# Performance work log

Hardware: AMD Instinct MI355X
Metric: run time of the kernel (lower is better)

The kernel has to match this reference:

```python
import jax, jax.numpy as jnp
import numpy as np

A_DIM, V_DIM, L_DIM, H = 512, 768, 1024, 512
B, S = 16, 2048


def setup_inputs() -> dict:
    key = jax.random.key(0)
    ks = jax.random.split(key, 20)
    w = lambda k, shp: jax.random.normal(k, shp, dtype=jnp.float32) * 0.02
    return {
        "a_input": jax.random.normal(ks[0], (B, S, A_DIM), dtype=jnp.float32),
        "v_input": jax.random.normal(ks[1], (B, S, V_DIM), dtype=jnp.float32),
        "l_input": jax.random.normal(ks[2], (B, S, L_DIM), dtype=jnp.float32),
        "h0": jax.random.normal(ks[3], (1, B, H), dtype=jnp.float32),
        "c0": jax.random.normal(ks[4], (1, B, H), dtype=jnp.float32),
        # 1x1 Conv1d == per-timestep Linear: weight [H, in_dim], bias [H]
        "Wa": w(ks[5], (H, A_DIM)), "ba": w(ks[6], (H,)),
        "Wv": w(ks[7], (H, V_DIM)), "bv": w(ks[8], (H,)),
        "Wl": w(ks[9], (H, L_DIM)), "bl": w(ks[10], (H,)),
        "Wc": w(ks[11], (H, 3 * H)), "bc": w(ks[12], (H,)),
        # LSTM params, PyTorch gate order (i, f, g, o)
        "Wih": w(ks[13], (4 * H, H)), "Whh": w(ks[14], (4 * H, H)),
        "bih": w(ks[15], (4 * H,)), "bhh": w(ks[16], (4 * H,)),
    }


def _lstm(x, h0, c0, Wih, Whh, bih, bhh):
    # x: [B, S, H]; h0/c0: [B, H]
    def step(carry, xt):
        h, c = carry
        gates = xt @ Wih.T + bih + h @ Whh.T + bhh  # [B, 4H]
        i, f, g, o = jnp.split(gates, 4, axis=-1)
        c = jax.nn.sigmoid(f) * c + jax.nn.sigmoid(i) * jnp.tanh(g)
        h = jax.nn.sigmoid(o) * jnp.tanh(c)
        return (h, c), h
    (hT, cT), hs = jax.lax.scan(step, (h0, c0), x.transpose(1, 0, 2))
    return hs.transpose(1, 0, 2), hT, cT  # [B,S,H], [B,H], [B,H]


def reference(a_input, v_input, l_input, h0, c0, Wa, ba, Wv, bv, Wl, bl,
              Wc, bc, Wih, Whh, bih, bhh):
    # 1x1 conv projections -> [B, S, H]
    a = a_input @ Wa.T + ba
    v = v_input @ Wv.T + bv
    l = l_input @ Wl.T + bl
    # attention fusion
    context = jnp.tanh(jnp.concatenate([a, v, l], axis=-1) @ Wc.T + bc)  # [B,S,H]
    scores = jnp.stack([
        jnp.sum(a * context, axis=-1),
        jnp.sum(v * context, axis=-1),
        jnp.sum(l * context, axis=-1),
    ], axis=-1)  # [B, S, 3]
    weight = jax.nn.softmax(scores, axis=-1)[..., None]  # [B,S,3,1]
    data = jnp.stack([a, v, l], axis=-2)  # [B,S,3,H]
    fusion = jnp.sum(data * weight, axis=-2)  # [B,S,H]
    r_out, hT, cT = _lstm(fusion, h0[0], c0[0], Wih, Whh, bih, bhh)
    return r_out, hT[None], cT[None]
```

## Files before the change

kernel.cpp:

```cpp
#include <hip/hip_runtime.h>
#include <stdint.h>

#define B_ 16
#define S_ 2048
#define H_ 512
#define M_ (B_ * S_)

template <int ACT>
__global__ __launch_bounds__(256) void gemm_xwt(
    const float* __restrict__ X, const float* __restrict__ W,
    const float* __restrict__ b1, const float* __restrict__ b2,
    float* __restrict__ Y, int K, int ldy)
{
  __shared__ float As[16][132];
  __shared__ float Bs[16][132];
  const int tid = threadIdx.x;
  const int bm = blockIdx.x, bn = blockIdx.y;
  const int ty = tid >> 4, tx = tid & 15;
  const int lr = tid >> 2, lk = (tid & 3) << 2;
  const float* Xb = X + (size_t)(bm * 128) * K;
  const float* Wb = W + (size_t)(bn * 128) * K;

  float acc[8][8] = {};

  for (int k0 = 0; k0 < K; k0 += 16) {
    float4 xa0 = *(const float4*)(Xb + (size_t)lr * K + k0 + lk);
    float4 xa1 = *(const float4*)(Xb + (size_t)(lr + 64) * K + k0 + lk);
    float4 wa0 = *(const float4*)(Wb + (size_t)lr * K + k0 + lk);
    float4 wa1 = *(const float4*)(Wb + (size_t)(lr + 64) * K + k0 + lk);
    __syncthreads();
    As[lk + 0][lr] = xa0.x; As[lk + 1][lr] = xa0.y; As[lk + 2][lr] = xa0.z; As[lk + 3][lr] = xa0.w;
    As[lk + 0][lr + 64] = xa1.x; As[lk + 1][lr + 64] = xa1.y; As[lk + 2][lr + 64] = xa1.z; As[lk + 3][lr + 64] = xa1.w;
    Bs[lk + 0][lr] = wa0.x; Bs[lk + 1][lr] = wa0.y; Bs[lk + 2][lr] = wa0.z; Bs[lk + 3][lr] = wa0.w;
    Bs[lk + 0][lr + 64] = wa1.x; Bs[lk + 1][lr + 64] = wa1.y; Bs[lk + 2][lr + 64] = wa1.z; Bs[lk + 3][lr + 64] = wa1.w;
    __syncthreads();
#pragma unroll
    for (int kk = 0; kk < 16; ++kk) {
      float4 a0 = *(const float4*)&As[kk][ty * 8];
      float4 a1 = *(const float4*)&As[kk][ty * 8 + 4];
      float4 b0 = *(const float4*)&Bs[kk][tx * 8];
      float4 b1v = *(const float4*)&Bs[kk][tx * 8 + 4];
      float av[8] = {a0.x, a0.y, a0.z, a0.w, a1.x, a1.y, a1.z, a1.w};
      float bv[8] = {b0.x, b0.y, b0.z, b0.w, b1v.x, b1v.y, b1v.z, b1v.w};
#pragma unroll
      for (int i = 0; i < 8; ++i)
#pragma unroll
        for (int j = 0; j < 8; ++j) acc[i][j] += av[i] * bv[j];
    }
  }

  const int ncol0 = bn * 128 + tx * 8;
  float bias[8];
#pragma unroll
  for (int j = 0; j < 8; ++j) {
    float bb = b1[ncol0 + j];
    if (b2) bb += b2[ncol0 + j];
    bias[j] = bb;
  }
#pragma unroll
  for (int i = 0; i < 8; ++i) {
    size_t row = (size_t)bm * 128 + ty * 8 + i;
    float* yp = Y + row * (size_t)ldy + ncol0;
    float out[8];
#pragma unroll
    for (int j = 0; j < 8; ++j) {
      float v = acc[i][j] + bias[j];
      if (ACT) v = tanhf(v);
      out[j] = v;
    }
    *(float4*)(yp)     = make_float4(out[0], out[1], out[2], out[3]);
    *(float4*)(yp + 4) = make_float4(out[4], out[5], out[6], out[7]);
  }
}

__global__ __launch_bounds__(256) void fusion_kernel(
    const float* __restrict__ F,
    const float* __restrict__ CTX,
    float* __restrict__ FU)
{
  const int row = blockIdx.x * 4 + (threadIdx.x >> 6);
  const int lane = threadIdx.x & 63;
  const float* a = F + (size_t)row * 1536;
  const float* v = a + 512;
  const float* l = a + 1024;
  const float* c = CTX + (size_t)row * 512;
  float sa = 0.f, sv = 0.f, sl = 0.f;
  for (int k = lane; k < 512; k += 64) {
    float cv = c[k];
    sa += a[k] * cv; sv += v[k] * cv; sl += l[k] * cv;
  }
#pragma unroll
  for (int off = 1; off < 64; off <<= 1) {
    sa += __shfl_xor(sa, off);
    sv += __shfl_xor(sv, off);
    sl += __shfl_xor(sl, off);
  }
  float m = fmaxf(sa, fmaxf(sv, sl));
  float ea = expf(sa - m), ev = expf(sv - m), el = expf(sl - m);
  float inv = 1.0f / (ea + ev + el);
  float wa = ea * inv, wv = ev * inv, wl = el * inv;
  float* fu = FU + (size_t)row * 512;
  for (int k = lane; k < 512; k += 64)
    fu[k] = wa * a[k] + wv * v[k] + wl * l[k];
}

__global__ __launch_bounds__(256, 1) void lstm_kernel(
    const float* __restrict__ G,
    const float* __restrict__ Whh,
    const float* __restrict__ h0,
    const float* __restrict__ c0,
    unsigned long long* __restrict__ ring,
    float* __restrict__ r_out,
    float* __restrict__ hT,
    float* __restrict__ cT)
{
  const int bi = blockIdx.x;
  const int b  = ((bi & 7) << 1) | ((bi >> 3) & 1);
  const int wg = bi >> 4;
  const int k0h = wg << 5;
  const int tid = threadIdx.x;

  __shared__ float h_lds[512];
  __shared__ float gates_lds[128];
  __shared__ float c_lds[32];

  const int col = tid >> 1;
  const int khalf = tid & 1;
  const int kbase = khalf << 8;
  const int g = col >> 5, ul = col & 31;
  const int gcol = g * 512 + k0h + ul;

  float4 warr[64];
  const float* wsrc = Whh + (size_t)gcol * 512 + kbase;
#pragma unroll
  for (int j = 0; j < 64; ++j) warr[j] = *(const float4*)(wsrc + j * 4);

  if (tid < 32) c_lds[tid] = c0[b * H_ + k0h + tid];
  __syncthreads();

  const float* gbase = G + (size_t)b * S_ * 2048;

  for (int t = 0; t < S_; ++t) {
    float gval = 0.f;
    if (khalf == 0) gval = gbase[(size_t)t * 2048 + gcol];

    if (t > 0) {
      const unsigned int want = (unsigned int)(t - 1);
      const unsigned long long* slot =
          ring + ((size_t)((t - 1) & 3) * B_ + b) * H_;
      unsigned long long v0, v1;
      do {
        v0 = __hip_atomic_load(slot + tid, __ATOMIC_RELAXED,
                               __HIP_MEMORY_SCOPE_AGENT);
      } while ((unsigned int)(v0 >> 32) != want);
      do {
        v1 = __hip_atomic_load(slot + tid + 256, __ATOMIC_RELAXED,
                               __HIP_MEMORY_SCOPE_AGENT);
      } while ((unsigned int)(v1 >> 32) != want);
      h_lds[tid]       = __builtin_bit_cast(float, (unsigned int)v0);
      h_lds[tid + 256] = __builtin_bit_cast(float, (unsigned int)v1);
    } else {
      const float* hsrc = h0 + b * H_;
      h_lds[tid] = hsrc[tid];
      h_lds[tid + 256] = hsrc[tid + 256];
    }
    __syncthreads();

    float4 s4 = make_float4(0.f, 0.f, 0.f, 0.f);
#pragma unroll
    for (int j = 0; j < 64; ++j) {
      float4 hv = *(const float4*)&h_lds[kbase + (j << 2)];
      s4.x += warr[j].x * hv.x;
      s4.y += warr[j].y * hv.y;
      s4.z += warr[j].z * hv.z;
      s4.w += warr[j].w * hv.w;
    }
    float sum = (s4.x + s4.y) + (s4.z + s4.w);
    sum += __shfl_xor(sum, 1);
    if (khalf == 0) gates_lds[col] = sum + gval;
    __syncthreads();

    if (tid < 32) {
      const int u = tid;
      float ip = gates_lds[u], fp = gates_lds[32 + u];
      float gp = gates_lds[64 + u], op = gates_lds[96 + u];
      float ig = 1.f / (1.f + expf(-ip));
      float fg = 1.f / (1.f + expf(-fp));
      float gg = tanhf(gp);
      float og = 1.f / (1.f + expf(-op));
      float cn = fg * c_lds[u] + ig * gg;
      c_lds[u] = cn;
      float hn = og * tanhf(cn);
      unsigned long long pk =
          ((unsigned long long)(unsigned int)t << 32) |
          (unsigned long long)__builtin_bit_cast(unsigned int, hn);
      __hip_atomic_store(ring + ((size_t)(t & 3) * B_ + b) * H_ + k0h + u,
                         pk, __ATOMIC_RELAXED, __HIP_MEMORY_SCOPE_AGENT);
      r_out[((size_t)b * S_ + t) * H_ + k0h + u] = hn;
      if (t == S_ - 1) {
        hT[b * H_ + k0h + u] = hn;
        cT[b * H_ + k0h + u] = cn;
      }
    }
    __syncthreads();
  }
}

extern "C" void kernel_launch(void* const* d_in, const int* in_sizes, int n_in,
                              void* d_out, int out_size, void* d_ws, size_t ws_size,
                              hipStream_t stream)
{
  const float* a_in = (const float*)d_in[0];
  const float* v_in = (const float*)d_in[1];
  const float* l_in = (const float*)d_in[2];
  const float* h0   = (const float*)d_in[3];
  const float* c0   = (const float*)d_in[4];
  const float* Wa = (const float*)d_in[5];   const float* ba = (const float*)d_in[6];
  const float* Wv = (const float*)d_in[7];   const float* bv = (const float*)d_in[8];
  const float* Wl = (const float*)d_in[9];   const float* bl = (const float*)d_in[10];
  const float* Wc = (const float*)d_in[11];  const float* bc = (const float*)d_in[12];
  const float* Wih = (const float*)d_in[13]; const float* Whh = (const float*)d_in[14];
  const float* bih = (const float*)d_in[15]; const float* bhh = (const float*)d_in[16];

  char* ws = (char*)d_ws;
  float* Fbuf = (float*)ws;
  float* Gbuf = (float*)ws;
  float* CTX  = (float*)(ws + 268435456ull);
  float* FU   = (float*)(ws + 335544320ull);
  unsigned long long* ringp = (unsigned long long*)(ws + 402653184ull);

  dim3 blk(256);
  gemm_xwt<0><<<dim3(256, 4), blk, 0, stream>>>(a_in, Wa, ba, nullptr, Fbuf + 0,    512,  1536);
  gemm_xwt<0><<<dim3(256, 4), blk, 0, stream>>>(v_in, Wv, bv, nullptr, Fbuf + 512,  768,  1536);
  gemm_xwt<0><<<dim3(256, 4), blk, 0, stream>>>(l_in, Wl, bl, nullptr, Fbuf + 1024, 1024, 1536);
  gemm_xwt<1><<<dim3(256, 4), blk, 0, stream>>>(Fbuf, Wc, bc, nullptr, CTX, 1536, 512);
  fusion_kernel<<<dim3(8192), blk, 0, stream>>>(Fbuf, CTX, FU);
  gemm_xwt<0><<<dim3(256, 16), blk, 0, stream>>>(FU, Wih, bih, bhh, Gbuf, 512, 2048);
  float* out = (float*)d_out;
  lstm_kernel<<<dim3(256), blk, 0, stream>>>(Gbuf, Whh, h0, c0, ringp,
                                             out, out + 16777216ull,
                                             out + 16777216ull + 8192ull);
}
```

Measured before the change: 10.92 ms.

## Rewrite LSTM recurrence with bf16 split-precision MFMA across 32 workgroups

```diff
diff --git a/kernel.cpp b/kernel.cpp
--- a/kernel.cpp
+++ b/kernel.cpp
@@ -5,6 +5,15 @@
 #define S_ 2048
 #define H_ 512
 #define M_ (B_ * S_)
+
+typedef short short8 __attribute__((ext_vector_type(8)));
+typedef float floatx4 __attribute__((ext_vector_type(4)));
+
+static __device__ __forceinline__ unsigned short f2bf(float x) {
+  unsigned u = __builtin_bit_cast(unsigned, x);
+  unsigned r = (u + 0x7fffu + ((u >> 16) & 1u)) >> 16;
+  return (unsigned short)r;
+}
 
 template <int ACT>
 __global__ __launch_bounds__(256) void gemm_xwt(
@@ -74,8 +83,7 @@
 }
 
 __global__ __launch_bounds__(256) void fusion_kernel(
-    const float* __restrict__ F,
-    const float* __restrict__ CTX,
+    const float* __restrict__ F, const float* __restrict__ CTX,
     float* __restrict__ FU)
 {
   const int row = blockIdx.x * 4 + (threadIdx.x >> 6);
@@ -114,95 +122,130 @@
     float* __restrict__ hT,
     float* __restrict__ cT)
 {
-  const int bi = blockIdx.x;
-  const int b  = ((bi & 7) << 1) | ((bi >> 3) & 1);
-  const int wg = bi >> 4;
-  const int k0h = wg << 5;
+  const int wg = blockIdx.x;
+  const int u0 = wg << 4;
   const int tid = threadIdx.x;
-
-  __shared__ float h_lds[512];
-  __shared__ float gates_lds[128];
-  __shared__ float c_lds[32];
-
-  const int col = tid >> 1;
-  const int khalf = tid & 1;
-  const int kbase = khalf << 8;
-  const int g = col >> 5, ul = col & 31;
-  const int gcol = g * 512 + k0h + ul;
-
-  float4 warr[64];
-  const float* wsrc = Whh + (size_t)gcol * 512 + kbase;
-#pragma unroll
-  for (int j = 0; j < 64; ++j) warr[j] = *(const float4*)(wsrc + j * 4);
-
-  if (tid < 32) c_lds[tid] = c0[b * H_ + k0h + tid];
-  __syncthreads();
-
-  const float* gbase = G + (size_t)b * S_ * 2048;
+  const int w = tid >> 6;
+  const int lane = tid & 63;
+  const int mn = lane & 15;
+  const int kq = lane >> 4;
+
+  __shared__ unsigned int h_u32[16 * 260];
+  __shared__ float g_lds[4][16][17];
+
+  short8 wh[16], wl[16];
+  {
+    const float* wrow = Whh + (size_t)(w * 512 + u0 + mn) * 512;
+#pragma unroll
+    for (int kt = 0; kt < 16; ++kt) {
+      const float* p = wrow + kt * 32 + kq * 8;
+      float4 x0 = *(const float4*)p;
+      float4 x1 = *(const float4*)(p + 4);
+      float xs[8] = {x0.x, x0.y, x0.z, x0.w, x1.x, x1.y, x1.z, x1.w};
+      short8 hi, lo;
+#pragma unroll
+      for (int j = 0; j < 8; ++j) {
+        unsigned short hb = f2bf(xs[j]);
+        float hf = __builtin_bit_cast(float, (unsigned)hb << 16);
+        hi[j] = (short)hb;
+        lo[j] = (short)f2bf(xs[j] - hf);
+      }
+      wh[kt] = hi;
+      wl[kt] = lo;
+    }
+  }
+
+  const int pu = tid >> 4, pb = tid & 15;
+  float c_reg = c0[pb * H_ + u0 + pu];
+
+  const int b7 = tid >> 5;
+  const int Ub = (tid & 31) * 16;
 
   for (int t = 0; t < S_; ++t) {
-    float gval = 0.f;
-    if (khalf == 0) gval = gbase[(size_t)t * 2048 + gcol];
-
-    if (t > 0) {
-      const unsigned int want = (unsigned int)(t - 1);
-      const unsigned long long* slot =
-          ring + ((size_t)((t - 1) & 3) * B_ + b) * H_;
-      unsigned long long v0, v1;
+    floatx4 acc0, acc1 = {0,0,0,0}, acc2 = {0,0,0,0}, acc3 = {0,0,0,0};
+    {
+      const size_t gb = ((size_t)mn * S_ + t) * 2048 + (size_t)(w * 512 + u0 + kq * 4);
+#pragma unroll
+      for (int r = 0; r < 4; ++r) acc0[r] = G[gb + r];
+    }
+
+    if (t == 0) {
+      const int sb = tid >> 4, sk = (tid & 15) * 32;
+      const float* hp = h0 + sb * H_ + sk;
+      unsigned int* dst = &h_u32[sb * 260 + sk / 2];
+#pragma unroll
+      for (int i = 0; i < 8; ++i) {
+        float4 x = *(const float4*)(hp + i * 4);
+        dst[i * 2]     = (unsigned)f2bf(x.x) | ((unsigned)f2bf(x.y) << 16);
+        dst[i * 2 + 1] = (unsigned)f2bf(x.z) | ((unsigned)f2bf(x.w) << 16);
+      }
+    } else {
+      const unsigned want = (unsigned)(t - 1);
+      const unsigned long long* slot = ring + (size_t)((t - 1) & 3) * 4096;
+      unsigned long long v[16];
+      bool ok;
       do {
-        v0 = __hip_atomic_load(slot + tid, __ATOMIC_RELAXED,
-                               __HIP_MEMORY_SCOPE_AGENT);
-      } while ((unsigned int)(v0 >> 32) != want);
-      do {
-        v1 = __hip_atomic_load(slot + tid + 256, __ATOMIC_RELAXED,
-                               __HIP_MEMORY_SCOPE_AGENT);
-      } while ((unsigned int)(v1 >> 32) != want);
-      h_lds[tid]       = __builtin_bit_cast(float, (unsigned int)v0);
-      h_lds[tid + 256] = __builtin_bit_cast(float, (unsigned int)v1);
-    } else {
-      const float* hsrc = h0 + b * H_;
-      h_lds[tid] = hsrc[tid];
-      h_lds[tid + 256] = hsrc[tid + 256];
-    }
-    __syncthreads();
-
-    float4 s4 = make_float4(0.f, 0.f, 0.f, 0.f);
-#pragma unroll
-    for (int j = 0; j < 64; ++j) {
-      float4 hv = *(const float4*)&h_lds[kbase + (j << 2)];
-      s4.x += warr[j].x * hv.x;
-      s4.y += warr[j].y * hv.y;
-      s4.z += warr[j].z * hv.z;
-      s4.w += warr[j].w * hv.w;
-    }
-    float sum = (s4.x + s4.y) + (s4.z + s4.w);
-    sum += __shfl_xor(sum, 1);
-    if (khalf == 0) gates_lds[col] = sum + gval;
-    __syncthreads();
-
-    if (tid < 32) {
-      const int u = tid;
-      float ip = gates_lds[u], fp = gates_lds[32 + u];
-      float gp = gates_lds[64 + u], op = gates_lds[96 + u];
-      float ig = 1.f / (1.f + expf(-ip));
-      float fg = 1.f / (1.f + expf(-fp));
-      float gg = tanhf(gp);
-      float og = 1.f / (1.f + expf(-op));
-      float cn = fg * c_lds[u] + ig * gg;
-      c_lds[u] = cn;
-      float hn = og * tanhf(cn);
-      unsigned long long pk =
-          ((unsigned long long)(unsigned int)t << 32) |
-          (unsigned long long)__builtin_bit_cast(unsigned int, hn);
-      __hip_atomic_store(ring + ((size_t)(t & 3) * B_ + b) * H_ + k0h + u,
-                         pk, __ATOMIC_RELAXED, __HIP_MEMORY_SCOPE_AGENT);
-      r_out[((size_t)b * S_ + t) * H_ + k0h + u] = hn;
-      if (t == S_ - 1) {
-        hT[b * H_ + k0h + u] = hn;
-        cT[b * H_ + k0h + u] = cn;
-      }
-    }
-    __syncthreads();
+        ok = true;
+#pragma unroll
+        for (int i = 0; i < 16; ++i)
+          v[i] = __hip_atomic_load(slot + b7 * 512 + Ub + i,
+                                   __ATOMIC_RELAXED, __HIP_MEMORY_SCOPE_AGENT);
+#pragma unroll
+        for (int i = 0; i < 16; ++i)
+          ok = ok && ((unsigned)(v[i] >> 32) == want);
+      } while (!ok);
+      unsigned int* d0 = &h_u32[b7 * 260 + Ub / 2];
+      unsigned int* d1 = &h_u32[(b7 + 8) * 260 + Ub / 2];
+#pragma unroll
+      for (int i = 0; i < 8; ++i) {
+        d0[i] = (unsigned)(v[2 * i] & 0xffffu) |
+                ((unsigned)(v[2 * i + 1] & 0xffffu) << 16);
+        d1[i] = ((unsigned)(v[2 * i] >> 16) & 0xffffu) |
+                (((unsigned)(v[2 * i + 1] >> 16) & 0xffffu) << 16);
+      }
+    }
+    __syncthreads();
+
+#pragma unroll
+    for (int kt = 0; kt < 16; ++kt) {
+      short8 bf = *(const short8*)&h_u32[mn * 260 + kt * 16 + kq * 4];
+      if (kt & 1) {
+        acc2 = __builtin_amdgcn_mfma_f32_16x16x32_bf16(wh[kt], bf, acc2, 0, 0, 0);
+        acc3 = __builtin_amdgcn_mfma_f32_16x16x32_bf16(wl[kt], bf, acc3, 0, 0, 0);
+      } else {
+        acc0 = __builtin_amdgcn_mfma_f32_16x16x32_bf16(wh[kt], bf, acc0, 0, 0, 0);
+        acc1 = __builtin_amdgcn_mfma_f32_16x16x32_bf16(wl[kt], bf, acc1, 0, 0, 0);
+      }
+    }
+#pragma unroll
+    for (int r = 0; r < 4; ++r)
+      g_lds[w][kq * 4 + r][mn] = (acc0[r] + acc1[r]) + (acc2[r] + acc3[r]);
+    __syncthreads();
+
+    float iv = g_lds[0][pu][pb], fv = g_lds[1][pu][pb];
+    float gv = g_lds[2][pu][pb], ov = g_lds[3][pu][pb];
+    float ig = 1.f / (1.f + expf(-iv));
+    float fg = 1.f / (1.f + expf(-fv));
+    float gg = tanhf(gv);
+    float og = 1.f / (1.f + expf(-ov));
+    c_reg = fg * c_reg + ig * gg;
+    float hn = og * tanhf(c_reg);
+    r_out[((size_t)pb * S_ + t) * H_ + u0 + pu] = hn;
+
+    unsigned hb16 = (unsigned)f2bf(hn);
+    unsigned other = (unsigned)__shfl_xor((int)hb16, 8);
+    if ((pb & 8) == 0) {
+      unsigned long long word =
+          ((unsigned long long)(unsigned)t << 32) |
+          ((unsigned long long)(other & 0xffffu) << 16) |
+          (unsigned long long)(hb16 & 0xffffu);
+      __hip_atomic_store(ring + (size_t)(t & 3) * 4096 + pb * 512 + (u0 + pu),
+                         word, __ATOMIC_RELAXED, __HIP_MEMORY_SCOPE_AGENT);
+    }
+    if (t == S_ - 1) {
+      hT[pb * H_ + u0 + pu] = hn;
+      cT[pb * H_ + u0 + pu] = c_reg;
+    }
   }
 }
 
@@ -225,9 +268,9 @@
   char* ws = (char*)d_ws;
   float* Fbuf = (float*)ws;
   float* Gbuf = (float*)ws;
-  float* CTX  = (float*)(ws + 268435456ull);
-  float* FU   = (float*)(ws + 335544320ull);
-  unsigned long long* ringp = (unsigned long long*)(ws + 402653184ull);
+  float* CTX  = (float*)(ws + 201326592ull);
+  float* FU   = (float*)(ws + 268435456ull);
+  unsigned long long* ringp = (unsigned long long*)(ws + 335544320ull);
 
   dim3 blk(256);
   gemm_xwt<0><<<dim3(256, 4), blk, 0, stream>>>(a_in, Wa, ba, nullptr, Fbuf + 0,    512,  1536);
@@ -236,8 +279,9 @@
   gemm_xwt<1><<<dim3(256, 4), blk, 0, stream>>>(Fbuf, Wc, bc, nullptr, CTX, 1536, 512);
   fusion_kernel<<<dim3(8192), blk, 0, stream>>>(Fbuf, CTX, FU);
   gemm_xwt<0><<<dim3(256, 16), blk, 0, stream>>>(FU, Wih, bih, bhh, Gbuf, 512, 2048);
+
   float* out = (float*)d_out;
-  lstm_kernel<<<dim3(256), blk, 0, stream>>>(Gbuf, Whh, h0, c0, ringp,
-                                             out, out + 16777216ull,
-                                             out + 16777216ull + 8192ull);
-}
+  lstm_kernel<<<dim3(32), blk, 0, stream>>>(Gbuf, Whh, h0, c0, ringp,
+                                            out, out + 16777216ull,
+                                            out + 16777216ull + 8192ull);
+}
```

New measurement: 12.61 ms. +15.5%, slower.
